# Kernel optimization log

Hardware: AMD Instinct MI355X
Metric: run time of the kernel (lower is better)

The kernel has to match this reference:

```python
import jax, jax.numpy as jnp
import numpy as np

N_NODES = 100000
D_GRAPH = 512    # graph_embedding_dim
D_ROUTE = 1024   # routes_embedding_dim
N_ROUTES = 16384
ROUTE_LEN = 32
N_BLOCKS = 3


def setup_inputs() -> dict:
    key = jax.random.key(0)
    ks = jax.random.split(key, 2 + 2 * N_BLOCKS)
    graph_embedding = jax.random.normal(ks[0], (N_NODES, D_GRAPH), dtype=jnp.float32)
    locations_idx = jax.random.randint(ks[1], (N_ROUTES, ROUTE_LEN), 0, N_NODES, dtype=jnp.int64)
    # Linear block chain: first block D_GRAPH->D_ROUTE, rest D_ROUTE->D_ROUTE, ReLU each
    dims = [D_GRAPH] + [D_ROUTE] * N_BLOCKS
    inp = {"graph_embedding": graph_embedding, "locations_idx": locations_idx}
    for i in range(N_BLOCKS):
        fan_in = dims[i]
        scale = 1.0 / np.sqrt(fan_in)
        inp[f"W{i}"] = jax.random.uniform(ks[2 + 2 * i], (fan_in, dims[i + 1]), jnp.float32, -scale, scale)
        inp[f"b{i}"] = jax.random.uniform(ks[3 + 2 * i], (dims[i + 1],), jnp.float32, -scale, scale)
    return inp


def reference(graph_embedding, locations_idx, W0, b0, W1, b1, W2, b2):
    # per-route gather: [R, L, D] then max over route positions -> [R, D]
    gathered = graph_embedding[locations_idx]          # [n_routes, route_len, d_graph]
    routes_emb = jnp.max(gathered, axis=1)             # [n_routes, d_graph]
    # linear block chain (Linear + ReLU per block)
    x = jax.nn.relu(routes_emb @ W0 + b0)
    x = jax.nn.relu(x @ W1 + b1)
    x = jax.nn.relu(x @ W2 + b2)
    return x
```

## Files before the change

### kernel.cpp

```cpp
#include <hip/hip_runtime.h>
#include <hip/hip_bf16.h>
#include <cstdint>


typedef __attribute__((ext_vector_type(8))) short          bf16x8;
typedef __attribute__((ext_vector_type(8))) unsigned short u16x8;
typedef __attribute__((ext_vector_type(4))) float          f32x4;

__device__ __forceinline__ unsigned short f2b_rne(float f) {
    union { float f; uint32_t i; } x; x.f = f;
    uint32_t lsb = (x.i >> 16) & 1u;
    return (unsigned short)((x.i + 0x7fffu + lsb) >> 16);
}

__device__ __forceinline__ void async_copy16(const void* gptr, void* lptr) {
    __builtin_amdgcn_global_load_lds(
        (const __attribute__((address_space(1))) unsigned int*)gptr,
        (__attribute__((address_space(3))) unsigned int*)lptr, 16, 0, 0);
}

__global__ void transpose_f32_bf16(const float* __restrict__ W,
                                   unsigned short* __restrict__ Wt,
                                   int K, int N)
{
    __shared__ float tile[32][33];
    const int n0 = blockIdx.x * 32;
    const int k0 = blockIdx.y * 32;
    const int tx = threadIdx.x & 31;
    const int ty = threadIdx.x >> 5;
#pragma unroll
    for (int i = 0; i < 32; i += 8)
        tile[ty + i][tx] = W[(size_t)(k0 + ty + i) * N + (n0 + tx)];
    __syncthreads();
#pragma unroll
    for (int i = 0; i < 32; i += 8)
        Wt[(size_t)(n0 + ty + i) * K + (k0 + tx)] = f2b_rne(tile[tx][ty + i]);
}

__global__ void gather_max_kernel(const float* __restrict__ graph,
                                  const int* __restrict__ idx32,
                                  unsigned short* __restrict__ routes)
{
    bool is64 = true;
#pragma unroll
    for (int k = 0; k < 64; k++) is64 &= (idx32[2 * k + 1] == 0);
    const int stride = is64 ? 64 : 32;
    const int step   = is64 ? 2  : 1;

    const int wave  = threadIdx.x >> 6;
    const int lane  = threadIdx.x & 63;
    const int route = (blockIdx.x * 4 + wave) * 2;
    const int col   = lane * 8;

    float m0[8], m1[8];
#pragma unroll
    for (int j = 0; j < 8; j++) { m0[j] = -INFINITY; m1[j] = -INFINITY; }

    const int* ip0 = idx32 + (size_t)route * stride;
    const int* ip1 = ip0 + stride;
#pragma unroll 4
    for (int l = 0; l < 32; l++) {
        const int n0 = ip0[l * step];
        const int n1 = ip1[l * step];
        const float4* p0 = reinterpret_cast<const float4*>(graph + (size_t)n0 * 512 + col);
        const float4* p1 = reinterpret_cast<const float4*>(graph + (size_t)n1 * 512 + col);
        float4 a0 = p0[0], a1 = p0[1];
        float4 b0 = p1[0], b1 = p1[1];
        m0[0] = fmaxf(m0[0], a0.x); m0[1] = fmaxf(m0[1], a0.y);
        m0[2] = fmaxf(m0[2], a0.z); m0[3] = fmaxf(m0[3], a0.w);
        m0[4] = fmaxf(m0[4], a1.x); m0[5] = fmaxf(m0[5], a1.y);
        m0[6] = fmaxf(m0[6], a1.z); m0[7] = fmaxf(m0[7], a1.w);
        m1[0] = fmaxf(m1[0], b0.x); m1[1] = fmaxf(m1[1], b0.y);
        m1[2] = fmaxf(m1[2], b0.z); m1[3] = fmaxf(m1[3], b0.w);
        m1[4] = fmaxf(m1[4], b1.x); m1[5] = fmaxf(m1[5], b1.y);
        m1[6] = fmaxf(m1[6], b1.z); m1[7] = fmaxf(m1[7], b1.w);
    }
    u16x8 o0, o1;
#pragma unroll
    for (int j = 0; j < 8; j++) { o0[j] = f2b_rne(m0[j]); o1[j] = f2b_rne(m1[j]); }
    *reinterpret_cast<u16x8*>(routes + (size_t)route * 512 + col)       = o0;
    *reinterpret_cast<u16x8*>(routes + (size_t)(route + 1) * 512 + col) = o1;
}

#define BM 128
#define BN 128
#define BK 32

template <typename OutT>
__global__ __launch_bounds__(256)
void gemm_bt_relu(const unsigned short* __restrict__ A,
                  const unsigned short* __restrict__ Bt,
                  const float* __restrict__ bias,
                  OutT* __restrict__ C,
                  int M, int N, int K)
{
    __shared__ unsigned short As[BM * BK];
    __shared__ unsigned short Bs[BN * BK];

    const int tid  = threadIdx.x;
    const int wave = tid >> 6;
    const int lane = tid & 63;
    const int quad = lane >> 4;
    const int l16  = lane & 15;
    const int wm   = (wave >> 1) * 64;
    const int wn   = (wave & 1) * 64;

    const int bm = blockIdx.y * BM;
    const int bn = blockIdx.x * BN;

    const int s0 = wave * 64 + lane;
    const int s1 = s0 + 256;
    const int r0 = s0 >> 2, c0 = (s0 & 3) ^ ((r0 >> 1) & 3);
    const int r1 = s1 >> 2, c1 = (s1 & 3) ^ ((r1 >> 1) & 3);

    const unsigned short* a0g = A  + (size_t)(bm + r0) * K + c0 * 8;
    const unsigned short* a1g = A  + (size_t)(bm + r1) * K + c1 * 8;
    const unsigned short* b0g = Bt + (size_t)(bn + r0) * K + c0 * 8;
    const unsigned short* b1g = Bt + (size_t)(bn + r1) * K + c1 * 8;
    unsigned short* a0l = As + s0 * 8;
    unsigned short* a1l = As + s1 * 8;
    unsigned short* b0l = Bs + s0 * 8;
    unsigned short* b1l = Bs + s1 * 8;

    f32x4 acc[4][4] = {};

    for (int k0 = 0; k0 < K; k0 += BK) {
        async_copy16(a0g + k0, a0l);
        async_copy16(a1g + k0, a1l);
        async_copy16(b0g + k0, b0l);
        async_copy16(b1g + k0, b1l);
        __syncthreads();

        bf16x8 a[4], b[4];
#pragma unroll
        for (int i = 0; i < 4; i++) {
            const int row = wm + i * 16 + l16;
            const int cp  = quad ^ ((row >> 1) & 3);
            a[i] = *reinterpret_cast<const bf16x8*>(As + row * BK + cp * 8);
        }
#pragma unroll
        for (int i = 0; i < 4; i++) {
            const int row = wn + i * 16 + l16;
            const int cp  = quad ^ ((row >> 1) & 3);
            b[i] = *reinterpret_cast<const bf16x8*>(Bs + row * BK + cp * 8);
        }

#pragma unroll
        for (int mi = 0; mi < 4; mi++)
#pragma unroll
            for (int ni = 0; ni < 4; ni++)
                acc[mi][ni] = __builtin_amdgcn_mfma_f32_16x16x32_bf16(
                    a[mi], b[ni], acc[mi][ni], 0, 0, 0);
        __syncthreads();
    }

#pragma unroll
    for (int ni = 0; ni < 4; ni++) {
        const int n  = bn + wn + ni * 16 + l16;
        const float bv = bias[n];
#pragma unroll
        for (int mi = 0; mi < 4; mi++) {
            const int mbase = bm + wm + mi * 16 + quad * 4;
#pragma unroll
            for (int r = 0; r < 4; r++) {
                float v = acc[mi][ni][r] + bv;
                v = fmaxf(v, 0.0f);
                if constexpr (sizeof(OutT) == 2)
                    C[(size_t)(mbase + r) * N + n] = (OutT)f2b_rne(v);
                else
                    C[(size_t)(mbase + r) * N + n] = (OutT)v;
            }
        }
    }
}

extern "C" void kernel_launch(void* const* d_in, const int* in_sizes, int n_in,
                              void* d_out, int out_size, void* d_ws, size_t ws_size,
                              hipStream_t stream)
{
    constexpr int N_ROUTES = 16384;
    constexpr int D_GRAPH  = 512;
    constexpr int D_ROUTE  = 1024;

    const float* graph = (const float*)d_in[0];
    const int*   idx   = (const int*)d_in[1];
    const float* W0    = (const float*)d_in[2];
    const float* b0    = (const float*)d_in[3];
    const float* W1    = (const float*)d_in[4];
    const float* b1    = (const float*)d_in[5];
    const float* W2    = (const float*)d_in[6];
    const float* b2    = (const float*)d_in[7];
    float*       out   = (float*)d_out;

    char* w = (char*)d_ws;
    unsigned short* Wt0    = (unsigned short*)w; w += (size_t)D_ROUTE * D_GRAPH * 2;
    unsigned short* Wt1    = (unsigned short*)w; w += (size_t)D_ROUTE * D_ROUTE * 2;
    unsigned short* Wt2    = (unsigned short*)w; w += (size_t)D_ROUTE * D_ROUTE * 2;
    unsigned short* routes = (unsigned short*)w; w += (size_t)N_ROUTES * D_GRAPH * 2;
    unsigned short* x1     = (unsigned short*)w; w += (size_t)N_ROUTES * D_ROUTE * 2;
    unsigned short* x2     = (unsigned short*)w; w += (size_t)N_ROUTES * D_ROUTE * 2;

    transpose_f32_bf16<<<dim3(D_ROUTE / 32, D_GRAPH / 32), 256, 0, stream>>>(W0, Wt0, D_GRAPH, D_ROUTE);
    transpose_f32_bf16<<<dim3(D_ROUTE / 32, D_ROUTE / 32), 256, 0, stream>>>(W1, Wt1, D_ROUTE, D_ROUTE);
    transpose_f32_bf16<<<dim3(D_ROUTE / 32, D_ROUTE / 32), 256, 0, stream>>>(W2, Wt2, D_ROUTE, D_ROUTE);

    gather_max_kernel<<<N_ROUTES / 8, 256, 0, stream>>>(graph, idx, routes);

    gemm_bt_relu<unsigned short><<<dim3(D_ROUTE / BN, N_ROUTES / BM), 256, 0, stream>>>(
        routes, Wt0, b0, x1, N_ROUTES, D_ROUTE, D_GRAPH);
    gemm_bt_relu<unsigned short><<<dim3(D_ROUTE / BN, N_ROUTES / BM), 256, 0, stream>>>(
        x1, Wt1, b1, x2, N_ROUTES, D_ROUTE, D_ROUTE);
    gemm_bt_relu<float><<<dim3(D_ROUTE / BN, N_ROUTES / BM), 256, 0, stream>>>(
        x2, Wt2, b2, out, N_ROUTES, D_ROUTE, D_ROUTE);
}
```

Before: 570.4 us.

## Gather from a bf16 copy of the graph and use BK=64 GEMM tiles

When the workspace is large enough, the whole graph embedding table is first converted to bf16. The gather-max kernel then reads half as many bytes per row and handles four routes per wave. Because rounding to bf16 preserves order, the max result is unchanged. Separately, the GEMM now uses a compile-time K and a 64-wide K tile with an 8-way XOR swizzle, which halves the number of barrier iterations. The trade-off is an extra full-table conversion pass and roughly 100 MB of extra workspace.

```diff
diff --git a/kernel.cpp b/kernel.cpp
--- a/kernel.cpp
+++ b/kernel.cpp
@@ -12,11 +12,26 @@
     uint32_t lsb = (x.i >> 16) & 1u;
     return (unsigned short)((x.i + 0x7fffu + lsb) >> 16);
 }
+__device__ __forceinline__ float b2f(unsigned short u) {
+    union { float f; uint32_t i; } x; x.i = ((uint32_t)u) << 16; return x.f;
+}
 
 __device__ __forceinline__ void async_copy16(const void* gptr, void* lptr) {
     __builtin_amdgcn_global_load_lds(
         (const __attribute__((address_space(1))) unsigned int*)gptr,
         (__attribute__((address_space(3))) unsigned int*)lptr, 16, 0, 0);
+}
+
+__global__ __launch_bounds__(256)
+void convert_f32_bf16(const float* __restrict__ in, unsigned short* __restrict__ out)
+{
+    const size_t i = ((size_t)blockIdx.x * 256 + threadIdx.x) * 8;
+    const float4* p = reinterpret_cast<const float4*>(in + i);
+    float4 v0 = p[0], v1 = p[1];
+    u16x8 o;
+    o[0] = f2b_rne(v0.x); o[1] = f2b_rne(v0.y); o[2] = f2b_rne(v0.z); o[3] = f2b_rne(v0.w);
+    o[4] = f2b_rne(v1.x); o[5] = f2b_rne(v1.y); o[6] = f2b_rne(v1.z); o[7] = f2b_rne(v1.w);
+    *reinterpret_cast<u16x8*>(out + i) = o;
 }
 
 __global__ void transpose_f32_bf16(const float* __restrict__ W,
@@ -37,9 +52,57 @@
         Wt[(size_t)(n0 + ty + i) * K + (k0 + tx)] = f2b_rne(tile[tx][ty + i]);
 }
 
-__global__ void gather_max_kernel(const float* __restrict__ graph,
-                                  const int* __restrict__ idx32,
-                                  unsigned short* __restrict__ routes)
+__global__ void gather_max_bf16(const unsigned short* __restrict__ graphb,
+                                const int* __restrict__ idx32,
+                                unsigned short* __restrict__ routes)
+{
+    bool is64 = true;
+#pragma unroll
+    for (int k = 0; k < 64; k++) is64 &= (idx32[2 * k + 1] == 0);
+    const int stride = is64 ? 64 : 32;
+    const int step   = is64 ? 2  : 1;
+
+    const int wave  = threadIdx.x >> 6;
+    const int lane  = threadIdx.x & 63;
+    const int route = (blockIdx.x * 4 + wave) * 4;
+    const int col   = lane * 8;
+
+    float m[4][8];
+#pragma unroll
+    for (int t = 0; t < 4; t++)
+#pragma unroll
+        for (int j = 0; j < 8; j++) m[t][j] = -INFINITY;
+
+    const int* ip = idx32 + (size_t)route * stride;
+#pragma unroll 2
+    for (int l = 0; l < 32; l++) {
+        u16x8 v[4];
+#pragma unroll
+        for (int t = 0; t < 4; t++) {
+            const int node = ip[t * stride + l * step];
+            v[t] = *reinterpret_cast<const u16x8*>(graphb + (size_t)node * 512 + col);
+        }
+#pragma unroll
+        for (int t = 0; t < 4; t++)
+#pragma unroll
+            for (int j = 0; j < 8; j++)
+                m[t][j] = fmaxf(m[t][j], b2f(v[t][j]));
+    }
+#pragma unroll
+    for (int t = 0; t < 4; t++) {
+        u16x8 o;
+#pragma unroll
+        for (int j = 0; j < 8; j++) {
+            union { float f; uint32_t i; } x; x.f = m[t][j];
+            o[j] = (unsigned short)(x.i >> 16);
+        }
+        *reinterpret_cast<u16x8*>(routes + (size_t)(route + t) * 512 + col) = o;
+    }
+}
+
+__global__ void gather_max_f32(const float* __restrict__ graph,
+                               const int* __restrict__ idx32,
+                               unsigned short* __restrict__ routes)
 {
     bool is64 = true;
 #pragma unroll
@@ -82,20 +145,17 @@
     *reinterpret_cast<u16x8*>(routes + (size_t)(route + 1) * 512 + col) = o1;
 }
 
-#define BM 128
-#define BN 128
-#define BK 32
-
-template <typename OutT>
+template <int K, typename OutT>
 __global__ __launch_bounds__(256)
 void gemm_bt_relu(const unsigned short* __restrict__ A,
                   const unsigned short* __restrict__ Bt,
                   const float* __restrict__ bias,
-                  OutT* __restrict__ C,
-                  int M, int N, int K)
-{
-    __shared__ unsigned short As[BM * BK];
-    __shared__ unsigned short Bs[BN * BK];
+                  OutT* __restrict__ C)
+{
+    constexpr int N  = 1024;
+    constexpr int BK = 64;
+    __shared__ unsigned short As[128 * BK];
+    __shared__ unsigned short Bs[128 * BK];
 
     const int tid  = threadIdx.x;
     const int wave = tid >> 6;
@@ -105,52 +165,56 @@
     const int wm   = (wave >> 1) * 64;
     const int wn   = (wave & 1) * 64;
 
-    const int bm = blockIdx.y * BM;
-    const int bn = blockIdx.x * BN;
-
-    const int s0 = wave * 64 + lane;
-    const int s1 = s0 + 256;
-    const int r0 = s0 >> 2, c0 = (s0 & 3) ^ ((r0 >> 1) & 3);
-    const int r1 = s1 >> 2, c1 = (s1 & 3) ^ ((r1 >> 1) & 3);
-
-    const unsigned short* a0g = A  + (size_t)(bm + r0) * K + c0 * 8;
-    const unsigned short* a1g = A  + (size_t)(bm + r1) * K + c1 * 8;
-    const unsigned short* b0g = Bt + (size_t)(bn + r0) * K + c0 * 8;
-    const unsigned short* b1g = Bt + (size_t)(bn + r1) * K + c1 * 8;
-    unsigned short* a0l = As + s0 * 8;
-    unsigned short* a1l = As + s1 * 8;
-    unsigned short* b0l = Bs + s0 * 8;
-    unsigned short* b1l = Bs + s1 * 8;
+    const int bm = blockIdx.y * 128;
+    const int bn = blockIdx.x * 128;
+
+    int sr[4], sc[4];
+    const unsigned short *ag[4], *bg[4];
+    unsigned short *al[4], *bl[4];
+#pragma unroll
+    for (int j = 0; j < 4; j++) {
+        const int s = wave * 64 + lane + j * 256;
+        const int r = s >> 3;
+        const int c = (s & 7) ^ (r & 7);
+        sr[j] = r; sc[j] = c;
+        ag[j] = A  + (size_t)(bm + r) * K + c * 8;
+        bg[j] = Bt + (size_t)(bn + r) * K + c * 8;
+        al[j] = As + s * 8;
+        bl[j] = Bs + s * 8;
+    }
 
     f32x4 acc[4][4] = {};
 
     for (int k0 = 0; k0 < K; k0 += BK) {
-        async_copy16(a0g + k0, a0l);
-        async_copy16(a1g + k0, a1l);
-        async_copy16(b0g + k0, b0l);
-        async_copy16(b1g + k0, b1l);
+#pragma unroll
+        for (int j = 0; j < 4; j++) async_copy16(ag[j] + k0, al[j]);
+#pragma unroll
+        for (int j = 0; j < 4; j++) async_copy16(bg[j] + k0, bl[j]);
         __syncthreads();
 
-        bf16x8 a[4], b[4];
-#pragma unroll
-        for (int i = 0; i < 4; i++) {
-            const int row = wm + i * 16 + l16;
-            const int cp  = quad ^ ((row >> 1) & 3);
-            a[i] = *reinterpret_cast<const bf16x8*>(As + row * BK + cp * 8);
-        }
-#pragma unroll
-        for (int i = 0; i < 4; i++) {
-            const int row = wn + i * 16 + l16;
-            const int cp  = quad ^ ((row >> 1) & 3);
-            b[i] = *reinterpret_cast<const bf16x8*>(Bs + row * BK + cp * 8);
-        }
-
-#pragma unroll
-        for (int mi = 0; mi < 4; mi++)
-#pragma unroll
-            for (int ni = 0; ni < 4; ni++)
-                acc[mi][ni] = __builtin_amdgcn_mfma_f32_16x16x32_bf16(
-                    a[mi], b[ni], acc[mi][ni], 0, 0, 0);
+#pragma unroll
+        for (int kk = 0; kk < 2; kk++) {
+            const int ch = kk * 4 + quad;
+            bf16x8 a[4], b[4];
+#pragma unroll
+            for (int i = 0; i < 4; i++) {
+                const int row = wm + i * 16 + l16;
+                a[i] = *reinterpret_cast<const bf16x8*>(
+                    As + row * BK + (ch ^ (row & 7)) * 8);
+            }
+#pragma unroll
+            for (int i = 0; i < 4; i++) {
+                const int row = wn + i * 16 + l16;
+                b[i] = *reinterpret_cast<const bf16x8*>(
+                    Bs + row * BK + (ch ^ (row & 7)) * 8);
+            }
+#pragma unroll
+            for (int mi = 0; mi < 4; mi++)
+#pragma unroll
+                for (int ni = 0; ni < 4; ni++)
+                    acc[mi][ni] = __builtin_amdgcn_mfma_f32_16x16x32_bf16(
+                        a[mi], b[ni], acc[mi][ni], 0, 0, 0);
+        }
         __syncthreads();
     }
 
@@ -179,6 +243,7 @@
                               hipStream_t stream)
 {
     constexpr int N_ROUTES = 16384;
+    constexpr int N_NODES  = 100000;
     constexpr int D_GRAPH  = 512;
     constexpr int D_ROUTE  = 1024;
 
@@ -199,17 +264,25 @@
     unsigned short* routes = (unsigned short*)w; w += (size_t)N_ROUTES * D_GRAPH * 2;
     unsigned short* x1     = (unsigned short*)w; w += (size_t)N_ROUTES * D_ROUTE * 2;
     unsigned short* x2     = (unsigned short*)w; w += (size_t)N_ROUTES * D_ROUTE * 2;
+    unsigned short* graphb = (unsigned short*)w;
+    const size_t need_bf16 = (size_t)(w - (char*)d_ws) + (size_t)N_NODES * D_GRAPH * 2;
+    const bool   use_bf16  = (ws_size >= need_bf16);
 
     transpose_f32_bf16<<<dim3(D_ROUTE / 32, D_GRAPH / 32), 256, 0, stream>>>(W0, Wt0, D_GRAPH, D_ROUTE);
     transpose_f32_bf16<<<dim3(D_ROUTE / 32, D_ROUTE / 32), 256, 0, stream>>>(W1, Wt1, D_ROUTE, D_ROUTE);
     transpose_f32_bf16<<<dim3(D_ROUTE / 32, D_ROUTE / 32), 256, 0, stream>>>(W2, Wt2, D_ROUTE, D_ROUTE);
 
-    gather_max_kernel<<<N_ROUTES / 8, 256, 0, stream>>>(graph, idx, routes);
-
-    gemm_bt_relu<unsigned short><<<dim3(D_ROUTE / BN, N_ROUTES / BM), 256, 0, stream>>>(
-        routes, Wt0, b0, x1, N_ROUTES, D_ROUTE, D_GRAPH);
-    gemm_bt_relu<unsigned short><<<dim3(D_ROUTE / BN, N_ROUTES / BM), 256, 0, stream>>>(
-        x1, Wt1, b1, x2, N_ROUTES, D_ROUTE, D_ROUTE);
-    gemm_bt_relu<float><<<dim3(D_ROUTE / BN, N_ROUTES / BM), 256, 0, stream>>>(
-        x2, Wt2, b2, out, N_ROUTES, D_ROUTE, D_ROUTE);
-}
+    if (use_bf16) {
+        convert_f32_bf16<<<(N_NODES * D_GRAPH / 8) / 256, 256, 0, stream>>>(graph, graphb);
+        gather_max_bf16<<<N_ROUTES / 16, 256, 0, stream>>>(graphb, idx, routes);
+    } else {
+        gather_max_f32<<<N_ROUTES / 8, 256, 0, stream>>>(graph, idx, routes);
+    }
+
+    gemm_bt_relu<512,  unsigned short><<<dim3(D_ROUTE / 128, N_ROUTES / 128), 256, 0, stream>>>(
+        routes, Wt0, b0, x1);
+    gemm_bt_relu<1024, unsigned short><<<dim3(D_ROUTE / 128, N_ROUTES / 128), 256, 0, stream>>>(
+        x1, Wt1, b1, x2);
+    gemm_bt_relu<1024, float><<<dim3(D_ROUTE / 128, N_ROUTES / 128), 256, 0, stream>>>(
+        x2, Wt2, b2, out);
+}
```

Measured after the change: 539.9 us. 1.06x faster.
